# Performance work log

Measured on AMD Instinct MI355X. Metric: run time of the kernel, lower is better.

Reference implementation:

```python
import jax, jax.numpy as jnp
import numpy as np

N_QUBITS = 8
N_QLAYERS = 2
D_MODEL = 8
NUM_HEADS = 2
DEPTH = D_MODEL // NUM_HEADS


def _apply_1q(state, U, wire):
    # state: (T, 2, 2, ..., 2); U: (2, 2) complex
    state = jnp.moveaxis(state, 1 + wire, -1)
    state = jnp.einsum('...b,ab->...a', state, U)
    return jnp.moveaxis(state, -1, 1 + wire)


def _apply_cnot(state, ctrl, tgt):
    s = jnp.moveaxis(state, (1 + ctrl, 1 + tgt), (-2, -1))
    s = jnp.concatenate([s[..., :1, :], s[..., 1:, ::-1]], axis=-2)
    return jnp.moveaxis(s, (-2, -1), (1 + ctrl, 1 + tgt))


def _z_signs(n):
    idx = jnp.arange(2 ** n)
    bits = (idx[:, None] >> jnp.arange(n - 1, -1, -1)[None, :]) & 1  # col i = qubit i
    return (1.0 - 2.0 * bits).astype(jnp.float32)  # (2^n, n)


def quantum_circuit(x, w):
    """AngleEmbedding(RX) + BasicEntanglerLayers(RX + CNOT ring) + PauliZ expvals.
    x: (T, n) float angles; w: (L, n) float weights -> (T, n) float expvals."""
    T, n = x.shape
    L = w.shape[0]
    # AngleEmbedding: RX(x_i)|0> = cos(x_i/2)|0> - i sin(x_i/2)|1>; product state
    h = 0.5 * x
    amps = jnp.stack([jnp.cos(h).astype(jnp.complex64),
                      (-1j) * jnp.sin(h).astype(jnp.complex64)], axis=-1)  # (T, n, 2)
    state = amps[:, 0, :]
    for i in range(1, n):
        state = (state[:, :, None] * amps[:, i, None, :]).reshape(T, -1)
    state = state.reshape((T,) + (2,) * n)
    for l in range(L):
        for i in range(n):
            th = 0.5 * w[l, i]
            cc = jnp.cos(th).astype(jnp.complex64)
            ss = (-1j) * jnp.sin(th).astype(jnp.complex64)
            U = jnp.stack([jnp.stack([cc, ss]), jnp.stack([ss, cc])])  # RX(w)
            state = _apply_1q(state, U, i)
        pairs = [(i, (i + 1) % n) for i in range(n)] if n > 2 else [(0, 1)]
        for c, t in pairs:
            state = _apply_cnot(state, c, t)
    probs = jnp.abs(state.reshape(T, -1)) ** 2  # (T, 2^n)
    return probs @ _z_signs(n)  # (T, n)


def setup_inputs() -> dict:
    key = jax.random.key(0)
    ks = jax.random.split(key, 8)
    B, S, d = 32, 1024, D_MODEL
    q = jax.random.normal(ks[0], (B, S, d), dtype=jnp.float32)
    k = jax.random.normal(ks[1], (B, S, d), dtype=jnp.float32)
    v = jax.random.normal(ks[2], (B, S, d), dtype=jnp.float32)
    mask = jnp.triu(jnp.ones((S, S), dtype=jnp.float32), k=1)[None, None]  # causal
    weights_q = jax.random.uniform(ks[3], (N_QLAYERS, N_QUBITS), dtype=jnp.float32, maxval=2 * np.pi)
    weights_k = jax.random.uniform(ks[4], (N_QLAYERS, N_QUBITS), dtype=jnp.float32, maxval=2 * np.pi)
    weights_v = jax.random.uniform(ks[5], (N_QLAYERS, N_QUBITS), dtype=jnp.float32, maxval=2 * np.pi)
    weights_dense = jax.random.uniform(ks[6], (N_QLAYERS, N_QUBITS), dtype=jnp.float32, maxval=2 * np.pi)
    return {"q": q, "k": k, "v": v, "mask": mask,
            "weights_q": weights_q, "weights_k": weights_k,
            "weights_v": weights_v, "weights_dense": weights_dense}


def reference(q, k, v, mask, weights_q, weights_k, weights_v, weights_dense):
    B, S, d = q.shape
    T = B * S
    # per-token quantum Q/K/V embeddings (batched over all B*S tokens)
    qe = quantum_circuit(q.reshape(T, d), weights_q).reshape(B, S, d)
    ke = quantum_circuit(k.reshape(T, d), weights_k).reshape(B, S, d)
    ve = quantum_circuit(v.reshape(T, d), weights_v).reshape(B, S, d)
    # split heads: (B, H, S, depth)
    def split(x):
        return x.reshape(B, S, NUM_HEADS, DEPTH).transpose(0, 2, 1, 3)
    qh, kh, vh = split(qe), split(ke), split(ve)
    scores = jnp.einsum('bhqd,bhkd->bhqk', qh, kh) / jnp.sqrt(jnp.float32(DEPTH))
    scores = scores + mask * (-1e9)
    attn = jax.nn.softmax(scores, axis=-1)
    ctx = jnp.einsum('bhqk,bhkd->bhqd', attn, vh)
    ctx = ctx.transpose(0, 2, 1, 3).reshape(B, S, d)
    out = quantum_circuit(ctx.reshape(T, d), weights_dense).reshape(B, S, d)
    return out, attn
```

## Files before the change

### kernel.cpp

```cpp
#include <hip/hip_runtime.h>

#define S_LEN 1024
#define BATCH 32
#define NHEAD 2
#define HDIM  4


#define TBL_STRIDE 256

__global__ __launch_bounds__(256)
void pauli_setup(const float* __restrict__ wq, const float* __restrict__ wk,
                 const float* __restrict__ wv, const float* __restrict__ wd,
                 float4* __restrict__ tables, int* __restrict__ counts)
{
    int blk = blockIdx.x;
    int set = blk >> 3, w = blk & 7;
    const float* wt = (set == 0) ? wq : (set == 1) ? wk : (set == 2) ? wv : wd;

    float c2[8], s2[8];
#pragma unroll
    for (int j = 0; j < 8; ++j) {
        float th = wt[8 + j];
        s2[j] = __sinf(th);
        c2[j] = __cosf(th);
    }

    unsigned X = 0u, Z = 1u << w;
    int sg0 = 0;
#pragma unroll
    for (int g = 7; g >= 0; --g) {
        int c = g, t = (g + 1) & 7;
        unsigned xc = (X >> c) & 1u, zt = (Z >> t) & 1u;
        unsigned xt = (X >> t) & 1u, zc = (Z >> c) & 1u;
        sg0 ^= (int)(xc & zt & (xt ^ zc ^ 1u));
        X ^= xc << t;
        Z ^= zt << c;
    }

    int tid = threadIdx.x;
    float coef = sg0 ? -1.0f : 1.0f;
    unsigned Xb = X;
    int k = 0;
#pragma unroll
    for (int j = 0; j < 8; ++j) {
        if ((Z >> j) & 1u) {
            int bit = (tid >> k) & 1;
            ++k;
            if (!((X >> j) & 1u)) {
                if (bit) { Xb |= 1u << j; coef *= s2[j]; }
                else     { coef *= c2[j]; }
            } else {
                if (bit) { Xb &= ~(1u << j); coef *= -s2[j]; }
                else     { coef *= c2[j]; }
            }
        }
    }
    bool valid = (tid < (1 << k));

    unsigned Xf = Xb, Zf = Z;
    int sg = 0;
#pragma unroll
    for (int g = 7; g >= 0; --g) {
        int c = g, t = (g + 1) & 7;
        unsigned xc = (Xf >> c) & 1u, zt = (Zf >> t) & 1u;
        unsigned xt = (Xf >> t) & 1u, zc = (Zf >> c) & 1u;
        sg ^= (int)(xc & zt & (xt ^ zc ^ 1u));
        Xf ^= xc << t;
        Zf ^= zt << c;
    }

    bool keep = valid && ((Xf & ~Zf) == 0u);
    if (sg ^ (__popc(Xf) & 1)) coef = -coef;
    unsigned zonly = Zf & ~Xf;
    unsigned ymask = Xf;

    __shared__ int wsum[4];
    int lane = tid & 63, wvx = tid >> 6;
    unsigned long long mb = __ballot((int)keep);
    if (lane == 0) wsum[wvx] = __popcll(mb);
    __syncthreads();
    int prefix = 0;
#pragma unroll
    for (int i = 0; i < 4; ++i)
        if (i < wvx) prefix += wsum[i];
    int pos = prefix + __popcll(mb & ((1ull << lane) - 1ull));
    if (keep) {
        float4 t4;
        t4.x = __int_as_float((int)zonly);
        t4.y = __int_as_float((int)ymask);
        t4.z = coef;
        t4.w = 0.0f;
        tables[blk * TBL_STRIDE + pos] = t4;
    }
    __syncthreads();
    if (tid == 0) counts[blk] = wsum[0] + wsum[1] + wsum[2] + wsum[3];
}

__global__ __launch_bounds__(256)
void qc_eval(const float* __restrict__ x0, const float* __restrict__ w0a,
             const float* __restrict__ x1, const float* __restrict__ w0b,
             const float* __restrict__ x2, const float* __restrict__ w0c,
             const float4* __restrict__ tables, const int* __restrict__ counts,
             float* __restrict__ o0, float* __restrict__ o1, float* __restrict__ o2,
             int rows_per_seg, int set_base)
{
    int gr = blockIdx.x * 256 + threadIdx.x;
    int seg = gr / rows_per_seg;
    int row = gr - seg * rows_per_seg;
    const float* x  = (seg == 0) ? x0 : (seg == 1) ? x1 : x2;
    const float* w0 = (seg == 0) ? w0a : (seg == 1) ? w0b : w0c;
    float*       o  = (seg == 0) ? o0 : (seg == 1) ? o1 : o2;
    int set = set_base + seg;

    const float4* xp = reinterpret_cast<const float4*>(x + (size_t)row * 8);
    float4 xa = xp[0], xb = xp[1];
    float cc[8], ss[8];
    {
        float a;
        a = xa.x + w0[0]; __sincosf(a, &ss[0], &cc[0]);
        a = xa.y + w0[1]; __sincosf(a, &ss[1], &cc[1]);
        a = xa.z + w0[2]; __sincosf(a, &ss[2], &cc[2]);
        a = xa.w + w0[3]; __sincosf(a, &ss[3], &cc[3]);
        a = xb.x + w0[4]; __sincosf(a, &ss[4], &cc[4]);
        a = xb.y + w0[5]; __sincosf(a, &ss[5], &cc[5]);
        a = xb.z + w0[6]; __sincosf(a, &ss[6], &cc[6]);
        a = xb.w + w0[7]; __sincosf(a, &ss[7], &cc[7]);
    }

    float res[8];
#pragma unroll
    for (int w = 0; w < 8; ++w) {
        int blk = set * 8 + w;
        int cnt = counts[blk];
        const float4* base = tables + blk * TBL_STRIDE;
        float acc = 0.0f;
        for (int t = 0; t < cnt; ++t) {
            float4 T = base[t];
            unsigned zm = (unsigned)__float_as_int(T.x);
            unsigned ym = (unsigned)__float_as_int(T.y);
            float v = T.z;
#pragma unroll
            for (int m = 0; m < 8; ++m) {
                float f = ((ym >> m) & 1u) ? ss[m]
                        : (((zm >> m) & 1u) ? cc[m] : 1.0f);
                v *= f;
            }
            acc += v;
        }
        res[w] = acc;
    }

    float4* op = reinterpret_cast<float4*>(o + (size_t)row * 8);
    op[0] = make_float4(res[0], res[1], res[2], res[3]);
    op[1] = make_float4(res[4], res[5], res[6], res[7]);
}

__global__ __launch_bounds__(256)
void attn_kernel(const float* qe, const float* __restrict__ ke,
                 const float* __restrict__ ve, float* __restrict__ attn,
                 float* ctx)
{
    __shared__ float kT[HDIM][S_LEN];
    __shared__ float vT[HDIM][S_LEN];

    int tid = threadIdx.x;
    int bid = blockIdx.x;
    int it  = bid & 15;
    int h   = (bid >> 4) & 1;
    int b   = bid >> 5;

    const float4* ke4 = reinterpret_cast<const float4*>(ke);
    const float4* ve4 = reinterpret_cast<const float4*>(ve);
    for (int j = tid; j < S_LEN; j += 256) {
        float4 kk = ke4[((size_t)b * S_LEN + j) * 2 + h];
        float4 vv = ve4[((size_t)b * S_LEN + j) * 2 + h];
        kT[0][j] = kk.x; kT[1][j] = kk.y; kT[2][j] = kk.z; kT[3][j] = kk.w;
        vT[0][j] = vv.x; vT[1][j] = vv.y; vT[2][j] = vv.z; vT[3][j] = vv.w;
    }
    __syncthreads();

    int lane = tid & 63;
    int wave = tid >> 6;
    int i0   = it * 64 + wave * 16;

    for (int rr = 0; rr < 16; ++rr) {
        int i = i0 + rr;
        const float* qrow = qe + ((size_t)b * S_LEN + i) * 8 + h * HDIM;
        float q0 = qrow[0], q1 = qrow[1], q2 = qrow[2], q3 = qrow[3];

        float sc[16];
        float mx = -3.0e38f;
#pragma unroll
        for (int t = 0; t < 16; ++t) {
            int j = t * 64 + lane;
            float s = q0 * kT[0][j] + q1 * kT[1][j] + q2 * kT[2][j] + q3 * kT[3][j];
            s *= 0.5f;
            s = (j <= i) ? s : -1.0e9f;
            sc[t] = s;
            mx = fmaxf(mx, s);
        }
#pragma unroll
        for (int m = 1; m < 64; m <<= 1) mx = fmaxf(mx, __shfl_xor(mx, m));

        float sum = 0.0f, pv0 = 0, pv1 = 0, pv2 = 0, pv3 = 0;
#pragma unroll
        for (int t = 0; t < 16; ++t) {
            int j = t * 64 + lane;
            float pe = __expf(sc[t] - mx);
            sc[t] = pe;
            sum += pe;
            pv0 += pe * vT[0][j];
            pv1 += pe * vT[1][j];
            pv2 += pe * vT[2][j];
            pv3 += pe * vT[3][j];
        }
#pragma unroll
        for (int m = 1; m < 64; m <<= 1) sum += __shfl_xor(sum, m);
        float inv = 1.0f / sum;

        size_t base = (((size_t)(b * NHEAD + h)) * S_LEN + i) * S_LEN;
#pragma unroll
        for (int t = 0; t < 16; ++t) attn[base + t * 64 + lane] = sc[t] * inv;

#pragma unroll
        for (int m = 1; m < 64; m <<= 1) {
            pv0 += __shfl_xor(pv0, m);
            pv1 += __shfl_xor(pv1, m);
            pv2 += __shfl_xor(pv2, m);
            pv3 += __shfl_xor(pv3, m);
        }
        if (lane == 0) {
            float* c = ctx + ((size_t)b * S_LEN + i) * 8 + h * HDIM;
            c[0] = pv0 * inv; c[1] = pv1 * inv; c[2] = pv2 * inv; c[3] = pv3 * inv;
        }
    }
}

extern "C" void kernel_launch(void* const* d_in, const int* in_sizes, int n_in,
                              void* d_out, int out_size, void* d_ws, size_t ws_size,
                              hipStream_t stream)
{
    const float* q  = (const float*)d_in[0];
    const float* k  = (const float*)d_in[1];
    const float* v  = (const float*)d_in[2];
    const float* wq = (const float*)d_in[4];
    const float* wk = (const float*)d_in[5];
    const float* wv = (const float*)d_in[6];
    const float* wd = (const float*)d_in[7];

    float* out  = (float*)d_out;
    float* attn = out + (size_t)BATCH * S_LEN * 8;

    float*  ws     = (float*)d_ws;
    float*  qe     = ws;
    float*  ke     = ws + 262144;
    float*  ve     = ws + 524288;
    float4* tables = (float4*)(ws + 786432);
    int*    counts = (int*)(ws + 786432 + 32768);

    const int rows = BATCH * S_LEN;

    pauli_setup<<<dim3(32), 256, 0, stream>>>(wq, wk, wv, wd, tables, counts);

    qc_eval<<<dim3(rows * 3 / 256), 256, 0, stream>>>(
        q, wq, k, wk, v, wv, tables, counts, qe, ke, ve, rows, 0);

    attn_kernel<<<dim3(BATCH * NHEAD * 16), 256, 0, stream>>>(qe, ke, ve, attn, qe);

    qc_eval<<<dim3(rows / 256), 256, 0, stream>>>(
        qe, wd, qe, wd, qe, wd, tables, counts, out, out, out, rows, 3);
}
```

Baseline: 109.8 us.

## Hold K/V in registers and drop softmax max pass in attention

Each lane now keeps its 16 key/value columns in registers instead of staging them in shared memory, which removes the LDS traffic and the block barrier. The max-reduction pass is dropped because the quantum embeddings are bounded expectation values, so the scores are small and exp cannot overflow; masked entries are set to zero directly. Attention probabilities are written with nontemporal stores to avoid polluting cache, and launch bounds ask for two blocks per CU. The register footprint rises to over 128 floats per thread, which may cost occupancy, and skipping the max subtraction relies on the scores staying bounded.

New measurement: 102.7 us. 6.5% less time.

```diff
diff --git a/kernel.cpp b/kernel.cpp
--- a/kernel.cpp
+++ b/kernel.cpp
@@ -155,64 +155,54 @@
     op[1] = make_float4(res[4], res[5], res[6], res[7]);
 }
 
-__global__ __launch_bounds__(256)
+__global__ __launch_bounds__(256, 2)
 void attn_kernel(const float* qe, const float* __restrict__ ke,
                  const float* __restrict__ ve, float* __restrict__ attn,
                  float* ctx)
 {
-    __shared__ float kT[HDIM][S_LEN];
-    __shared__ float vT[HDIM][S_LEN];
-
     int tid = threadIdx.x;
     int bid = blockIdx.x;
     int it  = bid & 15;
     int h   = (bid >> 4) & 1;
     int b   = bid >> 5;
-
+    int lane = tid & 63;
+    int wave = tid >> 6;
+
+    float kR0[16], kR1[16], kR2[16], kR3[16];
+    float vR0[16], vR1[16], vR2[16], vR3[16];
     const float4* ke4 = reinterpret_cast<const float4*>(ke);
     const float4* ve4 = reinterpret_cast<const float4*>(ve);
-    for (int j = tid; j < S_LEN; j += 256) {
+#pragma unroll
+    for (int t = 0; t < 16; ++t) {
+        int j = t * 64 + lane;
         float4 kk = ke4[((size_t)b * S_LEN + j) * 2 + h];
         float4 vv = ve4[((size_t)b * S_LEN + j) * 2 + h];
-        kT[0][j] = kk.x; kT[1][j] = kk.y; kT[2][j] = kk.z; kT[3][j] = kk.w;
-        vT[0][j] = vv.x; vT[1][j] = vv.y; vT[2][j] = vv.z; vT[3][j] = vv.w;
-    }
-    __syncthreads();
-
-    int lane = tid & 63;
-    int wave = tid >> 6;
-    int i0   = it * 64 + wave * 16;
-
+        kR0[t] = kk.x; kR1[t] = kk.y; kR2[t] = kk.z; kR3[t] = kk.w;
+        vR0[t] = vv.x; vR1[t] = vv.y; vR2[t] = vv.z; vR3[t] = vv.w;
+    }
+
+    int i0 = it * 64 + wave * 16;
+
+#pragma unroll 1
     for (int rr = 0; rr < 16; ++rr) {
         int i = i0 + rr;
         const float* qrow = qe + ((size_t)b * S_LEN + i) * 8 + h * HDIM;
-        float q0 = qrow[0], q1 = qrow[1], q2 = qrow[2], q3 = qrow[3];
-
-        float sc[16];
-        float mx = -3.0e38f;
+        float q0 = qrow[0] * 0.5f, q1 = qrow[1] * 0.5f;
+        float q2 = qrow[2] * 0.5f, q3 = qrow[3] * 0.5f;
+
+        float pe[16];
+        float sum = 0.0f, pv0 = 0, pv1 = 0, pv2 = 0, pv3 = 0;
 #pragma unroll
         for (int t = 0; t < 16; ++t) {
             int j = t * 64 + lane;
-            float s = q0 * kT[0][j] + q1 * kT[1][j] + q2 * kT[2][j] + q3 * kT[3][j];
-            s *= 0.5f;
-            s = (j <= i) ? s : -1.0e9f;
-            sc[t] = s;
-            mx = fmaxf(mx, s);
-        }
-#pragma unroll
-        for (int m = 1; m < 64; m <<= 1) mx = fmaxf(mx, __shfl_xor(mx, m));
-
-        float sum = 0.0f, pv0 = 0, pv1 = 0, pv2 = 0, pv3 = 0;
-#pragma unroll
-        for (int t = 0; t < 16; ++t) {
-            int j = t * 64 + lane;
-            float pe = __expf(sc[t] - mx);
-            sc[t] = pe;
-            sum += pe;
-            pv0 += pe * vT[0][j];
-            pv1 += pe * vT[1][j];
-            pv2 += pe * vT[2][j];
-            pv3 += pe * vT[3][j];
+            float s = q0 * kR0[t] + q1 * kR1[t] + q2 * kR2[t] + q3 * kR3[t];
+            float p = (j <= i) ? __expf(s) : 0.0f;
+            pe[t] = p;
+            sum += p;
+            pv0 += p * vR0[t];
+            pv1 += p * vR1[t];
+            pv2 += p * vR2[t];
+            pv3 += p * vR3[t];
         }
 #pragma unroll
         for (int m = 1; m < 64; m <<= 1) sum += __shfl_xor(sum, m);
@@ -220,7 +210,8 @@
 
         size_t base = (((size_t)(b * NHEAD + h)) * S_LEN + i) * S_LEN;
 #pragma unroll
-        for (int t = 0; t < 16; ++t) attn[base + t * 64 + lane] = sc[t] * inv;
+        for (int t = 0; t < 16; ++t)
+            __builtin_nontemporal_store(pe[t] * inv, &attn[base + t * 64 + lane]);
 
 #pragma unroll
         for (int m = 1; m < 64; m <<= 1) {
```
